# Kernel tuning notes

Measured on AMD Instinct MI355X. Metric: run time of the kernel, lower is better.

## Reference

```python
import jax, jax.numpy as jnp
import numpy as np

N_NODES = 50000
N_EDGES = 800000
D_IN = 128
D_HID = 128
D_OUT = 128


def setup_inputs() -> dict:
    key = jax.random.key(0)
    ks = jax.random.split(key, 10)
    x = jax.random.normal(ks[0], (N_NODES, D_IN), dtype=jnp.float32)
    edge_index = jax.random.randint(ks[1], (2, N_EDGES), 0, N_NODES, dtype=jnp.int64)
    edge_index_inter = jax.random.randint(ks[2], (2, N_EDGES), 0, N_NODES, dtype=jnp.int64)
    # nn.Linear-style params: W [out, in], b [out]
    def linear(k, fan_in, fan_out):
        k1, k2 = jax.random.split(k)
        bound = 1.0 / np.sqrt(fan_in)
        W = jax.random.uniform(k1, (fan_out, fan_in), minval=-bound, maxval=bound, dtype=jnp.float32)
        b = jax.random.uniform(k2, (fan_out,), minval=-bound, maxval=bound, dtype=jnp.float32)
        return W, b
    W1, b1 = linear(ks[3], D_IN, D_HID)
    W2, b2 = linear(ks[4], D_HID, D_HID)
    W3, b3 = linear(ks[5], D_HID, D_OUT)
    return {"x": x, "W1": W1, "b1": b1, "W2": W2, "b2": b2, "W3": W3, "b3": b3,
            "edge_index": edge_index, "edge_index_inter": edge_index_inter}


def _gnn_layer(h, W, b, src, dst, n_nodes):
    # message: lin(x_j - x_i); x_j = source features, x_i = target features (PyG convention)
    msg = (h[src] - h[dst]) @ W.T + b          # [E, out]
    # aggr='add': scatter-add messages into target nodes
    return jax.ops.segment_sum(msg, dst, num_segments=n_nodes)  # [N, out]


def reference(x, W1, b1, W2, b2, W3, b3, edge_index, edge_index_inter):
    src, dst = edge_index[0], edge_index[1]
    n = x.shape[0]
    h = _gnn_layer(x, W1, b1, src, dst, n)
    h = _gnn_layer(h, W2, b2, src, dst, n)
    return _gnn_layer(h, W3, b3, src, dst, n)
```

## Files before the change

kernel.cpp:

```cpp
#include <hip/hip_runtime.h>

#define N_NODES 50000
#define N_EDGES 800000
#define D 128
#define TN 8
#define TSTR 136
#define SCAN_BLOCKS 196
#define ZROW N_NODES

typedef __attribute__((ext_vector_type(8))) short bf16x8;
typedef __attribute__((ext_vector_type(4))) float f32x4;

__device__ __forceinline__ unsigned short f32_to_bf16_rne(float f) {
    unsigned u = __float_as_uint(f);
    u += 0x7fffu + ((u >> 16) & 1u);
    return (unsigned short)(u >> 16);
}

__device__ __forceinline__ float bflo(unsigned u) { return __uint_as_float(u << 16); }
__device__ __forceinline__ float bfhi(unsigned u) { return __uint_as_float(u & 0xffff0000u); }

__device__ __forceinline__ void acc8(uint4 r, float* a) {
    a[0] += bflo(r.x); a[1] += bfhi(r.x);
    a[2] += bflo(r.y); a[3] += bfhi(r.y);
    a[4] += bflo(r.z); a[5] += bfhi(r.z);
    a[6] += bflo(r.w); a[7] += bfhi(r.w);
}

__device__ __forceinline__ void gather16x8(const unsigned short* __restrict__ hb,
                                           int myidx, int i, int rowid2, int d8,
                                           float* a0, float* a1) {
    int si[8];
    uint4 rr[8];
#pragma unroll
    for (int u = 0; u < 8; ++u) si[u] = __shfl(myidx, i + 2 * u + rowid2, 32);
#pragma unroll
    for (int u = 0; u < 8; ++u) rr[u] = *(const uint4*)(hb + (size_t)si[u] * D + 8 * d8);
#pragma unroll
    for (int u = 0; u < 8; ++u) acc8(rr[u], (u & 1) ? a1 : a0);
}

__device__ __forceinline__ void gather_node(const unsigned short* __restrict__ hb,
                                            const unsigned short* __restrict__ esrc,
                                            int beg, int deg, int idx0,
                                            int l32, int rowid2, int d8,
                                            float* out) {
    float a0[8] = {0.f, 0.f, 0.f, 0.f, 0.f, 0.f, 0.f, 0.f};
    float a1[8] = {0.f, 0.f, 0.f, 0.f, 0.f, 0.f, 0.f, 0.f};
    int myidx = idx0;
    int base = 0;
    while (true) {
        const int cnt = min(deg - base, 32);
        for (int i = 0; i < cnt; i += 16)
            gather16x8(hb, myidx, i, rowid2, d8, a0, a1);
        base += 32;
        if (base >= deg) break;
        myidx = ZROW;
        if (l32 < deg - base) myidx = (int)esrc[beg + base + l32];
    }
#pragma unroll
    for (int k = 0; k < 8; ++k) {
        float s = a0[k] + a1[k];
        s += __shfl_xor(s, 16, 64);
        out[k] = s;
    }
}

__global__ void prep_kernel(const int* __restrict__ dst, int* __restrict__ counts,
                            unsigned short* __restrict__ rank,
                            const float* __restrict__ x, unsigned short* __restrict__ xb,
                            unsigned short* __restrict__ h1, unsigned short* __restrict__ h2) {
    const int t = blockIdx.x * blockDim.x + threadIdx.x;
    if (t < N_EDGES) {
        rank[t] = (unsigned short)atomicAdd(&counts[dst[t]], 1);
    }
    {
        const float4 v0 = *(const float4*)(x + (size_t)t * 8);
        const float4 v1 = *(const float4*)(x + (size_t)t * 8 + 4);
        uint4 p;
        p.x = (unsigned)f32_to_bf16_rne(v0.x) | ((unsigned)f32_to_bf16_rne(v0.y) << 16);
        p.y = (unsigned)f32_to_bf16_rne(v0.z) | ((unsigned)f32_to_bf16_rne(v0.w) << 16);
        p.z = (unsigned)f32_to_bf16_rne(v1.x) | ((unsigned)f32_to_bf16_rne(v1.y) << 16);
        p.w = (unsigned)f32_to_bf16_rne(v1.z) | ((unsigned)f32_to_bf16_rne(v1.w) << 16);
        *(uint4*)(xb + (size_t)t * 8) = p;
    }
    if (blockIdx.x == 0 && threadIdx.x < 48) {
        const int rowsel = threadIdx.x >> 4;
        const int off = threadIdx.x & 15;
        unsigned short* zp = (rowsel == 0) ? xb : (rowsel == 1) ? h1 : h2;
        *(uint4*)(zp + (size_t)ZROW * D + off * 8) = make_uint4(0u, 0u, 0u, 0u);
    }
}

__global__ void block_sum_kernel(const int* __restrict__ counts, int* __restrict__ bsum) {
    __shared__ int red[256];
    const int tid = threadIdx.x;
    const int i = blockIdx.x * 256 + tid;
    red[tid] = (i < N_NODES) ? counts[i] : 0;
    __syncthreads();
    for (int s = 128; s > 0; s >>= 1) {
        if (tid < s) red[tid] += red[tid + s];
        __syncthreads();
    }
    if (tid == 0) bsum[blockIdx.x] = red[0];
}

__global__ void bsum_scan_kernel(const int* __restrict__ bsum,
                                 int* __restrict__ bpre,
                                 int* __restrict__ offsets) {
    __shared__ int s[256];
    const int tid = threadIdx.x;
    const int v = (tid < SCAN_BLOCKS) ? bsum[tid] : 0;
    s[tid] = v;
    __syncthreads();
    for (int off = 1; off < 256; off <<= 1) {
        int a = (tid >= off) ? s[tid - off] : 0;
        __syncthreads();
        s[tid] += a;
        __syncthreads();
    }
    bpre[tid] = s[tid] - v;
    if (tid == 255) offsets[N_NODES] = s[255];
}

__global__ void offsets_wfrag_kernel(const int* __restrict__ counts,
                                     const int* __restrict__ bpre,
                                     int* __restrict__ offsets,
                                     const float* __restrict__ W1,
                                     const float* __restrict__ W2,
                                     const float* __restrict__ W3,
                                     unsigned short* __restrict__ Wb) {
    if (blockIdx.x < SCAN_BLOCKS) {
        __shared__ int s[256];
        const int tid = threadIdx.x;
        const int i = blockIdx.x * 256 + tid;
        const int v = (i < N_NODES) ? counts[i] : 0;
        s[tid] = v;
        __syncthreads();
        for (int off = 1; off < 256; off <<= 1) {
            int a = (tid >= off) ? s[tid - off] : 0;
            __syncthreads();
            s[tid] += a;
            __syncthreads();
        }
        const int excl = s[tid] - v + bpre[blockIdx.x];
        if (i < N_NODES) offsets[i] = excl;
    } else {
        const int unit = (blockIdx.x - SCAN_BLOCKS) * 2 + (threadIdx.x >> 7);
        const int w = unit >> 7;
        const int o = unit & 127;
        const int k = threadIdx.x & 127;
        const float* W = (w == 0) ? W1 : (w == 1) ? W2 : W3;
        const unsigned short v = f32_to_bf16_rne(W[o * D + k]);
        const int nt = o >> 4, n = o & 15;
        const int kc = k >> 5, kr = k & 31, quad = kr >> 3, j = kr & 7;
        const int lane = quad * 16 + n;
        Wb[(((size_t)w * 8 + nt) * 4 + kc) * 512 + lane * 8 + j] = v;
    }
}

__global__ void fill_kernel(const int* __restrict__ src, const int* __restrict__ dst,
                            const unsigned short* __restrict__ rank,
                            const int* __restrict__ offsets,
                            unsigned short* __restrict__ esrc) {
    int e = blockIdx.x * blockDim.x + threadIdx.x;
    if (e < N_EDGES) {
        esrc[offsets[dst[e]] + (int)rank[e]] = (unsigned short)src[e];
    }
}

template <bool OUT_BF16>
__global__ __launch_bounds__(128) void gnn_layer_kernel(
    const unsigned short* __restrict__ hb,
    const int* __restrict__ offsets,
    const unsigned short* __restrict__ esrc,
    const unsigned short* __restrict__ Wb,
    const float* __restrict__ bias,
    float* __restrict__ outf,
    unsigned short* __restrict__ outb) {

    __shared__ __align__(16) unsigned short tb[16][TSTR];
    __shared__ float degf[TN];

    const int tid = threadIdx.x;
    const int wave = tid >> 6;
    const int lane = tid & 63;
    const int half = lane >> 5;
    const int l32 = lane & 31;
    const int rowid2 = (lane >> 4) & 1;
    const int d8 = lane & 15;
    const int vbase = blockIdx.x * TN;

    const int j0 = wave * 4 + half * 2;
    const int v0 = vbase + j0;

    const int begA = offsets[v0];
    const int begB = offsets[v0 + 1];
    const int degA = begB - begA;
    const int degB = offsets[v0 + 2] - begB;

    int idxA = ZROW, idxB = ZROW;
    if (l32 < min(degA, 32)) idxA = (int)esrc[begA + l32];
    if (l32 < min(degB, 32)) idxB = (int)esrc[begB + l32];

    float sA[8], sB[8];
    gather_node(hb, esrc, begA, degA, idxA, l32, rowid2, d8, sA);
    gather_node(hb, esrc, begB, degB, idxB, l32, rowid2, d8, sB);

    {
        const int vv = v0 + rowid2;
        const float dv = (float)(rowid2 ? degB : degA);
        const uint4 r = *(const uint4*)(hb + (size_t)vv * D + 8 * d8);
        float t[8];
#pragma unroll
        for (int k = 0; k < 8; ++k) t[k] = rowid2 ? sB[k] : sA[k];
        t[0] -= dv * bflo(r.x); t[1] -= dv * bfhi(r.x);
        t[2] -= dv * bflo(r.y); t[3] -= dv * bfhi(r.y);
        t[4] -= dv * bflo(r.z); t[5] -= dv * bfhi(r.z);
        t[6] -= dv * bflo(r.w); t[7] -= dv * bfhi(r.w);
        uint4 p;
        p.x = (unsigned)f32_to_bf16_rne(t[0]) | ((unsigned)f32_to_bf16_rne(t[1]) << 16);
        p.y = (unsigned)f32_to_bf16_rne(t[2]) | ((unsigned)f32_to_bf16_rne(t[3]) << 16);
        p.z = (unsigned)f32_to_bf16_rne(t[4]) | ((unsigned)f32_to_bf16_rne(t[5]) << 16);
        p.w = (unsigned)f32_to_bf16_rne(t[6]) | ((unsigned)f32_to_bf16_rne(t[7]) << 16);
        *(uint4*)&tb[j0 + rowid2][8 * d8] = p;
        if (d8 == 0) degf[j0 + rowid2] = dv;
    }
    __syncthreads();

    const int n16 = lane & 15;
    const int quad = lane >> 4;

    bf16x8 afrag[4];
#pragma unroll
    for (int kc = 0; kc < 4; ++kc)
        afrag[kc] = *(const bf16x8*)&tb[n16][kc * 32 + quad * 8];

#pragma unroll
    for (int i = 0; i < 4; ++i) {
        const int nt = wave * 4 + i;
        f32x4 acc = {0.f, 0.f, 0.f, 0.f};
#pragma unroll
        for (int kc = 0; kc < 4; ++kc) {
            const bf16x8 bfrag = *(const bf16x8*)&Wb[((nt * 4 + kc) * 64 + lane) * 8];
            acc = __builtin_amdgcn_mfma_f32_16x16x32_bf16(afrag[kc], bfrag, acc, 0, 0, 0);
        }
        if (quad < 2) {
            const int o = nt * 16 + n16;
            const float bo = bias[o];
#pragma unroll
            for (int r = 0; r < 4; ++r) {
                const int m = quad * 4 + r;
                const float val = acc[r] + degf[m] * bo;
                if (OUT_BF16)
                    outb[(size_t)(vbase + m) * D + o] = f32_to_bf16_rne(val);
                else
                    outf[(size_t)(vbase + m) * D + o] = val;
            }
        }
    }
}

extern "C" void kernel_launch(void* const* d_in, const int* in_sizes, int n_in,
                              void* d_out, int out_size, void* d_ws, size_t ws_size,
                              hipStream_t stream) {
    const float* x  = (const float*)d_in[0];
    const float* W1 = (const float*)d_in[1];
    const float* b1 = (const float*)d_in[2];
    const float* W2 = (const float*)d_in[3];
    const float* b2 = (const float*)d_in[4];
    const float* W3 = (const float*)d_in[5];
    const float* b3 = (const float*)d_in[6];
    const int*   ei = (const int*)d_in[7];

    const int* src = ei;
    const int* dst = ei + N_EDGES;
    float* out = (float*)d_out;

    const size_t HSLAB = (size_t)(N_NODES + 2) * D * 2;
    char* ws = (char*)d_ws;
    int* counts  = (int*)ws;                          ws += 204800;
    int* offsets = (int*)ws;                          ws += 204800;
    int* bsum    = (int*)ws;                          ws += 1024;
    int* bpre    = (int*)ws;                          ws += 1024;
    unsigned short* rank = (unsigned short*)ws;       ws += (size_t)N_EDGES * 2;
    unsigned short* esrc = (unsigned short*)ws;       ws += (size_t)N_EDGES * 2;
    unsigned short* Wb = (unsigned short*)ws;         ws += 3 * 16384 * 2;
    unsigned short* xb = (unsigned short*)ws;         ws += HSLAB;
    unsigned short* h1 = (unsigned short*)ws;         ws += HSLAB;
    unsigned short* h2 = (unsigned short*)ws;

    hipMemsetAsync(counts, 0, N_NODES * sizeof(int), stream);
    prep_kernel<<<(N_EDGES + 255) / 256, 256, 0, stream>>>(dst, counts, rank, x, xb, h1, h2);
    block_sum_kernel<<<SCAN_BLOCKS, 256, 0, stream>>>(counts, bsum);
    bsum_scan_kernel<<<1, 256, 0, stream>>>(bsum, bpre, offsets);
    offsets_wfrag_kernel<<<SCAN_BLOCKS + 192, 256, 0, stream>>>(counts, bpre, offsets,
                                                                W1, W2, W3, Wb);
    fill_kernel<<<(N_EDGES + 255) / 256, 256, 0, stream>>>(src, dst, rank, offsets, esrc);

    const int blocks = N_NODES / TN;

    gnn_layer_kernel<true ><<<blocks, 128, 0, stream>>>(xb, offsets, esrc, Wb,          b1, nullptr, h1);
    gnn_layer_kernel<true ><<<blocks, 128, 0, stream>>>(h1, offsets, esrc, Wb + 16384,  b2, nullptr, h2);
    gnn_layer_kernel<false><<<blocks, 128, 0, stream>>>(h2, offsets, esrc, Wb + 32768,  b3, out, nullptr);
}
```

Baseline: 254.6 us.

## Merge weight conversion into prep, single-block scan, and 16-node layer tiles

Weight bf16 fragment packing moves into the prep kernel as extra blocks. The three-kernel block-sum/scan/offset sequence becomes one 1024-thread single-block scan over chunks of 49 counts, which cuts two kernel launches. The layer kernel now processes 16 nodes per 256-thread block, so all 16 MFMA rows carry real nodes instead of half being padding, and each wave computes two output tiles. The single-block scan is serial per thread and may be slower than the parallel multi-block version.

```diff
diff --git a/kernel.cpp b/kernel.cpp
--- a/kernel.cpp
+++ b/kernel.cpp
@@ -3,9 +3,9 @@
 #define N_NODES 50000
 #define N_EDGES 800000
 #define D 128
-#define TN 8
+#define TN 16
 #define TSTR 136
-#define SCAN_BLOCKS 196
+#define EDGE_BLOCKS 3125
 #define ZROW N_NODES
 
 typedef __attribute__((ext_vector_type(8))) short bf16x8;
@@ -69,11 +69,24 @@
 __global__ void prep_kernel(const int* __restrict__ dst, int* __restrict__ counts,
                             unsigned short* __restrict__ rank,
                             const float* __restrict__ x, unsigned short* __restrict__ xb,
-                            unsigned short* __restrict__ h1, unsigned short* __restrict__ h2) {
+                            unsigned short* __restrict__ h1, unsigned short* __restrict__ h2,
+                            const float* __restrict__ W1, const float* __restrict__ W2,
+                            const float* __restrict__ W3, unsigned short* __restrict__ Wb) {
+    if (blockIdx.x >= EDGE_BLOCKS) {
+        const int unit = (blockIdx.x - EDGE_BLOCKS) * 2 + (threadIdx.x >> 7);
+        const int w = unit >> 7;
+        const int o = unit & 127;
+        const int k = threadIdx.x & 127;
+        const float* W = (w == 0) ? W1 : (w == 1) ? W2 : W3;
+        const unsigned short v = f32_to_bf16_rne(W[o * D + k]);
+        const int nt = o >> 4, n = o & 15;
+        const int kc = k >> 5, kr = k & 31, quad = kr >> 3, j = kr & 7;
+        const int lane = quad * 16 + n;
+        Wb[(((size_t)w * 8 + nt) * 4 + kc) * 512 + lane * 8 + j] = v;
+        return;
+    }
     const int t = blockIdx.x * blockDim.x + threadIdx.x;
-    if (t < N_EDGES) {
-        rank[t] = (unsigned short)atomicAdd(&counts[dst[t]], 1);
-    }
+    rank[t] = (unsigned short)atomicAdd(&counts[dst[t]], 1);
     {
         const float4 v0 = *(const float4*)(x + (size_t)t * 8);
         const float4 v1 = *(const float4*)(x + (size_t)t * 8 + 4);
@@ -92,70 +105,28 @@
     }
 }
 
-__global__ void block_sum_kernel(const int* __restrict__ counts, int* __restrict__ bsum) {
-    __shared__ int red[256];
+#define SCAN_CHUNK 49
+__global__ __launch_bounds__(1024) void scan_kernel(const int* __restrict__ counts,
+                                                    int* __restrict__ offsets) {
+    __shared__ int ssum[1024];
     const int tid = threadIdx.x;
-    const int i = blockIdx.x * 256 + tid;
-    red[tid] = (i < N_NODES) ? counts[i] : 0;
+    const int beg = tid * SCAN_CHUNK;
+    int s = 0;
+    const int rend = min(beg + SCAN_CHUNK, N_NODES);
+    for (int i = beg; i < rend; ++i) s += counts[i];
+    ssum[tid] = s;
     __syncthreads();
-    for (int s = 128; s > 0; s >>= 1) {
-        if (tid < s) red[tid] += red[tid + s];
+    for (int off = 1; off < 1024; off <<= 1) {
+        int a = (tid >= off) ? ssum[tid - off] : 0;
         __syncthreads();
-    }
-    if (tid == 0) bsum[blockIdx.x] = red[0];
-}
-
-__global__ void bsum_scan_kernel(const int* __restrict__ bsum,
-                                 int* __restrict__ bpre,
-                                 int* __restrict__ offsets) {
-    __shared__ int s[256];
-    const int tid = threadIdx.x;
-    const int v = (tid < SCAN_BLOCKS) ? bsum[tid] : 0;
-    s[tid] = v;
-    __syncthreads();
-    for (int off = 1; off < 256; off <<= 1) {
-        int a = (tid >= off) ? s[tid - off] : 0;
+        ssum[tid] += a;
         __syncthreads();
-        s[tid] += a;
-        __syncthreads();
-    }
-    bpre[tid] = s[tid] - v;
-    if (tid == 255) offsets[N_NODES] = s[255];
-}
-
-__global__ void offsets_wfrag_kernel(const int* __restrict__ counts,
-                                     const int* __restrict__ bpre,
-                                     int* __restrict__ offsets,
-                                     const float* __restrict__ W1,
-                                     const float* __restrict__ W2,
-                                     const float* __restrict__ W3,
-                                     unsigned short* __restrict__ Wb) {
-    if (blockIdx.x < SCAN_BLOCKS) {
-        __shared__ int s[256];
-        const int tid = threadIdx.x;
-        const int i = blockIdx.x * 256 + tid;
-        const int v = (i < N_NODES) ? counts[i] : 0;
-        s[tid] = v;
-        __syncthreads();
-        for (int off = 1; off < 256; off <<= 1) {
-            int a = (tid >= off) ? s[tid - off] : 0;
-            __syncthreads();
-            s[tid] += a;
-            __syncthreads();
-        }
-        const int excl = s[tid] - v + bpre[blockIdx.x];
-        if (i < N_NODES) offsets[i] = excl;
-    } else {
-        const int unit = (blockIdx.x - SCAN_BLOCKS) * 2 + (threadIdx.x >> 7);
-        const int w = unit >> 7;
-        const int o = unit & 127;
-        const int k = threadIdx.x & 127;
-        const float* W = (w == 0) ? W1 : (w == 1) ? W2 : W3;
-        const unsigned short v = f32_to_bf16_rne(W[o * D + k]);
-        const int nt = o >> 4, n = o & 15;
-        const int kc = k >> 5, kr = k & 31, quad = kr >> 3, j = kr & 7;
-        const int lane = quad * 16 + n;
-        Wb[(((size_t)w * 8 + nt) * 4 + kc) * 512 + lane * 8 + j] = v;
+    }
+    int run = ssum[tid] - s;
+    const int wend = min(beg + SCAN_CHUNK, N_NODES + 1);
+    for (int i = beg; i < wend; ++i) {
+        offsets[i] = run;
+        if (i < N_NODES) run += counts[i];
     }
 }
 
@@ -170,7 +141,7 @@
 }
 
 template <bool OUT_BF16>
-__global__ __launch_bounds__(128) void gnn_layer_kernel(
+__global__ __launch_bounds__(256) void gnn_layer_kernel(
     const unsigned short* __restrict__ hb,
     const int* __restrict__ offsets,
     const unsigned short* __restrict__ esrc,
@@ -179,7 +150,7 @@
     float* __restrict__ outf,
     unsigned short* __restrict__ outb) {
 
-    __shared__ __align__(16) unsigned short tb[16][TSTR];
+    __shared__ __align__(16) unsigned short tb[TN][TSTR];
     __shared__ float degf[TN];
 
     const int tid = threadIdx.x;
@@ -237,26 +208,24 @@
         afrag[kc] = *(const bf16x8*)&tb[n16][kc * 32 + quad * 8];
 
 #pragma unroll
-    for (int i = 0; i < 4; ++i) {
-        const int nt = wave * 4 + i;
+    for (int i = 0; i < 2; ++i) {
+        const int nt = wave * 2 + i;
         f32x4 acc = {0.f, 0.f, 0.f, 0.f};
 #pragma unroll
         for (int kc = 0; kc < 4; ++kc) {
             const bf16x8 bfrag = *(const bf16x8*)&Wb[((nt * 4 + kc) * 64 + lane) * 8];
             acc = __builtin_amdgcn_mfma_f32_16x16x32_bf16(afrag[kc], bfrag, acc, 0, 0, 0);
         }
-        if (quad < 2) {
-            const int o = nt * 16 + n16;
-            const float bo = bias[o];
-#pragma unroll
-            for (int r = 0; r < 4; ++r) {
-                const int m = quad * 4 + r;
-                const float val = acc[r] + degf[m] * bo;
-                if (OUT_BF16)
-                    outb[(size_t)(vbase + m) * D + o] = f32_to_bf16_rne(val);
-                else
-                    outf[(size_t)(vbase + m) * D + o] = val;
-            }
+        const int o = nt * 16 + n16;
+        const float bo = bias[o];
+#pragma unroll
+        for (int r = 0; r < 4; ++r) {
+            const int m = quad * 4 + r;
+            const float val = acc[r] + degf[m] * bo;
+            if (OUT_BF16)
+                outb[(size_t)(vbase + m) * D + o] = f32_to_bf16_rne(val);
+            else
+                outf[(size_t)(vbase + m) * D + o] = val;
         }
     }
 }
@@ -281,8 +250,6 @@
     char* ws = (char*)d_ws;
     int* counts  = (int*)ws;                          ws += 204800;
     int* offsets = (int*)ws;                          ws += 204800;
-    int* bsum    = (int*)ws;                          ws += 1024;
-    int* bpre    = (int*)ws;                          ws += 1024;
     unsigned short* rank = (unsigned short*)ws;       ws += (size_t)N_EDGES * 2;
     unsigned short* esrc = (unsigned short*)ws;       ws += (size_t)N_EDGES * 2;
     unsigned short* Wb = (unsigned short*)ws;         ws += 3 * 16384 * 2;
@@ -291,16 +258,14 @@
     unsigned short* h2 = (unsigned short*)ws;
 
     hipMemsetAsync(counts, 0, N_NODES * sizeof(int), stream);
-    prep_kernel<<<(N_EDGES + 255) / 256, 256, 0, stream>>>(dst, counts, rank, x, xb, h1, h2);
-    block_sum_kernel<<<SCAN_BLOCKS, 256, 0, stream>>>(counts, bsum);
-    bsum_scan_kernel<<<1, 256, 0, stream>>>(bsum, bpre, offsets);
-    offsets_wfrag_kernel<<<SCAN_BLOCKS + 192, 256, 0, stream>>>(counts, bpre, offsets,
-                                                                W1, W2, W3, Wb);
+    prep_kernel<<<EDGE_BLOCKS + 192, 256, 0, stream>>>(dst, counts, rank, x, xb, h1, h2,
+                                                       W1, W2, W3, Wb);
+    scan_kernel<<<1, 1024, 0, stream>>>(counts, offsets);
     fill_kernel<<<(N_EDGES + 255) / 256, 256, 0, stream>>>(src, dst, rank, offsets, esrc);
 
     const int blocks = N_NODES / TN;
 
-    gnn_layer_kernel<true ><<<blocks, 128, 0, stream>>>(xb, offsets, esrc, Wb,          b1, nullptr, h1);
-    gnn_layer_kernel<true ><<<blocks, 128, 0, stream>>>(h1, offsets, esrc, Wb + 16384,  b2, nullptr, h2);
-    gnn_layer_kernel<false><<<blocks, 128, 0, stream>>>(h2, offsets, esrc, Wb + 32768,  b3, out, nullptr);
-}
+    gnn_layer_kernel<true ><<<blocks, 256, 0, stream>>>(xb, offsets, esrc, Wb,          b1, nullptr, h1);
+    gnn_layer_kernel<true ><<<blocks, 256, 0, stream>>>(h1, offsets, esrc, Wb + 16384,  b2, nullptr, h2);
+    gnn_layer_kernel<false><<<blocks, 256, 0, stream>>>(h2, offsets, esrc, Wb + 32768,  b3, out, nullptr);
+}
```

Result: slower. 303.9 us (+19.3%).
